# Optimization experiments

Measured on AMD Instinct MI355X. Metric: run time of the kernel, lower is better.

The kernel has to match this reference:

```python
import jax, jax.numpy as jnp
import numpy as np

N, F = 16384, 32
H1, H2, D1, D2 = 64, 64, 32, 1


def setup_inputs() -> dict:
    key = jax.random.key(0)
    ks = jax.random.split(key, 10)
    x = jax.random.normal(ks[0], (N, F), dtype=jnp.float32)
    # pre-normalized adjacency (GCNConv expects D^-1/2 A D^-1/2); mimic with uniform/N
    a = jax.random.uniform(ks[1], (N, N), dtype=jnp.float32) / N
    # glorot-ish scaled params
    W1 = jax.random.normal(ks[2], (F, H1), dtype=jnp.float32) * (1.0 / np.sqrt(F))
    b1 = jnp.zeros((H1,), dtype=jnp.float32)
    W2 = jax.random.normal(ks[3], (H1, H2), dtype=jnp.float32) * (1.0 / np.sqrt(H1))
    b2 = jnp.zeros((H2,), dtype=jnp.float32)
    Wd1 = jax.random.normal(ks[4], (H2, D1), dtype=jnp.float32) * (1.0 / np.sqrt(H2))
    bd1 = jnp.zeros((D1,), dtype=jnp.float32)
    Wd2 = jax.random.normal(ks[5], (D1, D2), dtype=jnp.float32) * (1.0 / np.sqrt(D1))
    bd2 = jnp.zeros((D2,), dtype=jnp.float32)
    return {"x": x, "a": a, "W1": W1, "b1": b1, "W2": W2, "b2": b2,
            "Wd1": Wd1, "bd1": bd1, "Wd2": Wd2, "bd2": bd2}


def reference(x, a, W1, b1, W2, b2, Wd1, bd1, Wd2, bd2):
    # GCNConv: relu(a @ (x @ W) + b)   (a is pre-normalized)
    g1 = jax.nn.relu(a @ (x @ W1) + b1)   # [N, 64]
    g2 = jax.nn.relu(a @ (g1 @ W2) + b2)  # [N, 64]
    d3 = jax.nn.relu(g2 @ Wd1 + bd1)      # [N, 32]
    return d3 @ Wd2 + bd2                 # [N, 1]
```

## Files before the change

### kernel.cpp

```cpp
#include <hip/hip_runtime.h>
#include <hip/hip_bf16.h>


typedef __bf16 bf16x8 __attribute__((ext_vector_type(8)));
typedef float  f32x16 __attribute__((ext_vector_type(16)));
typedef float  f32x4v __attribute__((ext_vector_type(4)));
typedef int    i32x4  __attribute__((ext_vector_type(4)));

#define NNODE 16384
#define KDIM  16384
#define HCOL  64

__device__ inline i32x4 pack8(f32x4v a, f32x4v b){
  bf16x8 t;
  t[0]=(__bf16)a[0]; t[1]=(__bf16)a[1]; t[2]=(__bf16)a[2]; t[3]=(__bf16)a[3];
  t[4]=(__bf16)b[0]; t[5]=(__bf16)b[1]; t[6]=(__bf16)b[2]; t[7]=(__bf16)b[3];
  return __builtin_bit_cast(i32x4, t);
}

__global__ __launch_bounds__(128) void gcn_layer_kernel(
    const float* __restrict__ A,
    const __bf16* __restrict__ Ht,
    const float* __restrict__ bias,
    float* __restrict__ G)
{
  __shared__ i32x4 sA[2*2*256];
  __shared__ i32x4 sH[2*2*512];

  const int tid  = threadIdx.x;
  const int lane = tid & 63;
  const int kw   = tid >> 6;
  const int row0 = blockIdx.x * 32;

  const int rA0  = lane >> 3;
  const int ccA  = lane & 7;
  const int swzA = ccA ^ rA0;
  const int r    = lane & 31;
  const int hsub = lane >> 5;
  const int xs   = lane & 7;

  const size_t k0base = (size_t)kw * 8192;

  f32x4v ra[8]; i32x4 rh[8];

  const float* pA0 = A + (size_t)(row0 + rA0) * KDIM + k0base + (size_t)ccA*8;
  const i32x4* pH0 = (const i32x4*)Ht + (size_t)rA0 * (KDIM/8) + k0base/8 + ccA;

  auto stage_load = [&](int t){
    const float* pA = pA0 + (size_t)t*64;
    #pragma unroll
    for (int pi=0; pi<4; ++pi){
      const float* p = pA + (size_t)pi*8*KDIM;
      ra[2*pi]   = __builtin_nontemporal_load((const f32x4v*)p);
      ra[2*pi+1] = __builtin_nontemporal_load((const f32x4v*)(p+4));
    }
    const i32x4* pH = pH0 + (size_t)t*8;
    #pragma unroll
    for (int pi=0; pi<8; ++pi)
      rh[pi] = pH[(size_t)pi*8*(KDIM/8)];
  };

  auto stage_write = [&](int buf){
    i32x4* dA = &sA[(kw*2+buf)*256];
    #pragma unroll
    for (int pi=0; pi<4; ++pi)
      dA[(rA0 + pi*8)*8 + swzA] = pack8(ra[2*pi], ra[2*pi+1]);
    i32x4* dH = &sH[(kw*2+buf)*512];
    #pragma unroll
    for (int pi=0; pi<8; ++pi)
      dH[(rA0 + pi*8)*8 + swzA] = rh[pi];
  };

  f32x16 acc0 = {}; f32x16 acc1 = {};

  auto compute = [&](int buf){
    const i32x4* bA = &sA[(kw*2+buf)*256];
    const i32x4* bH = &sH[(kw*2+buf)*512];
    #pragma unroll
    for (int kk=0; kk<4; ++kk){
      int c = (kk*2 + hsub) ^ xs;
      bf16x8 a  = __builtin_bit_cast(bf16x8, bA[r*8 + c]);
      bf16x8 b0 = __builtin_bit_cast(bf16x8, bH[r*8 + c]);
      bf16x8 b1 = __builtin_bit_cast(bf16x8, bH[(r+32)*8 + c]);
      acc0 = __builtin_amdgcn_mfma_f32_32x32x16_bf16(a, b0, acc0, 0,0,0);
      acc1 = __builtin_amdgcn_mfma_f32_32x32x16_bf16(a, b1, acc1, 0,0,0);
    }
  };

  stage_load(0);
  stage_write(0);
  stage_load(1);

  #pragma unroll 1
  for (int t=0; t<127; ++t){
    int nx = t+2; if (nx > 127) nx = 127;
    compute(t&1);
    stage_write((t+1)&1);
    stage_load(nx);
  }
  compute(1);

  __syncthreads();

  float* red = (float*)sA;
  if (kw == 1){
    #pragma unroll
    for (int j=0; j<16; ++j){
      int rr = (j&3) + 8*(j>>2) + 4*hsub;
      red[rr*64 + r]      = acc0[j];
      red[rr*64 + 32 + r] = acc1[j];
    }
  }
  __syncthreads();
  if (kw == 0){
    #pragma unroll
    for (int j=0; j<16; ++j){
      int rr = (j&3) + 8*(j>>2) + 4*hsub;
      float v0 = acc0[j] + red[rr*64 + r]      + bias[r];
      float v1 = acc1[j] + red[rr*64 + 32 + r] + bias[32 + r];
      G[(size_t)(row0 + rr)*HCOL + r]      = fmaxf(v0, 0.f);
      G[(size_t)(row0 + rr)*HCOL + 32 + r] = fmaxf(v1, 0.f);
    }
  }
}

template<int F>
__global__ __launch_bounds__(128) void proj_T_kernel(
    const float* __restrict__ in,
    const float* __restrict__ W,
    __bf16* __restrict__ out)
{
  constexpr int FP = F + 4;
  __shared__ float sWt[64*FP];
  __shared__ short sOut[64*136];

  int tid = threadIdx.x;
  for (int e = tid; e < 64*F; e += 128){
    int h = e / F, j = e - h*F;
    sWt[h*FP + j] = W[j*64 + h];
  }
  __syncthreads();

  const size_t n = (size_t)blockIdx.x*128 + tid;
  float rowv[F];
  #pragma unroll
  for (int j=0; j<F; j+=4){
    f32x4v v = *(const f32x4v*)(in + n*F + j);
    rowv[j]=v[0]; rowv[j+1]=v[1]; rowv[j+2]=v[2]; rowv[j+3]=v[3];
  }
  #pragma unroll
  for (int h=0; h<64; ++h){
    float s = 0.f;
    #pragma unroll
    for (int j=0; j<F; j+=4){
      f32x4v w = *(const f32x4v*)&sWt[h*FP + j];
      s += rowv[j]*w[0] + rowv[j+1]*w[1] + rowv[j+2]*w[2] + rowv[j+3]*w[3];
    }
    sOut[h*136 + tid] = __builtin_bit_cast(short, (__bf16)s);
  }
  __syncthreads();

  const size_t n0 = (size_t)blockIdx.x*128;
  #pragma unroll
  for (int pi=0; pi<8; ++pi){
    int p = pi*128 + tid;
    int h = p >> 4, cc = p & 15;
    i32x4 v = *(const i32x4*)&sOut[h*136 + cc*8];
    *(i32x4*)(out + (size_t)h*NNODE + n0 + cc*8) = v;
  }
}

__global__ __launch_bounds__(256) void tail_kernel(
    const float* __restrict__ g2,
    const float* __restrict__ Wd1,
    const float* __restrict__ bd1,
    const float* __restrict__ Wd2,
    const float* __restrict__ bd2,
    float* __restrict__ outp)
{
  __shared__ float sW[64*32];
  __shared__ float sb1[32], sw2[32];
  int tid = threadIdx.x;
  for (int e=tid; e<2048; e+=256) sW[e] = Wd1[e];
  if (tid < 32){ sb1[tid] = bd1[tid]; sw2[tid] = Wd2[tid]; }
  __syncthreads();

  size_t n = (size_t)blockIdx.x*256 + tid;
  float rv[64];
  #pragma unroll
  for (int j=0;j<64;j+=4){
    f32x4v v = *(const f32x4v*)(g2 + n*64 + j);
    rv[j]=v[0]; rv[j+1]=v[1]; rv[j+2]=v[2]; rv[j+3]=v[3];
  }
  float o = 0.f;
  #pragma unroll
  for (int c=0;c<32;++c){
    float s = sb1[c];
    #pragma unroll
    for (int j=0;j<64;++j) s += rv[j]*sW[j*32 + c];
    o += fmaxf(s, 0.f) * sw2[c];
  }
  outp[n] = o + bd2[0];
}

extern "C" void kernel_launch(void* const* d_in, const int* in_sizes, int n_in,
                              void* d_out, int out_size, void* d_ws, size_t ws_size,
                              hipStream_t stream)
{
  const float* x   = (const float*)d_in[0];
  const float* a   = (const float*)d_in[1];
  const float* W1  = (const float*)d_in[2];
  const float* b1  = (const float*)d_in[3];
  const float* W2  = (const float*)d_in[4];
  const float* b2  = (const float*)d_in[5];
  const float* Wd1 = (const float*)d_in[6];
  const float* bd1 = (const float*)d_in[7];
  const float* Wd2 = (const float*)d_in[8];
  const float* bd2 = (const float*)d_in[9];
  float* outp = (float*)d_out;

  char* ws = (char*)d_ws;
  __bf16* Ht1 = (__bf16*)(ws);
  __bf16* Ht2 = (__bf16*)(ws + (2u<<20));
  float*  g1  = (float*)(ws + (4u<<20));
  float*  g2  = (float*)(ws + (8u<<20));

  proj_T_kernel<32><<<128, 128, 0, stream>>>(x,  W1, Ht1);
  gcn_layer_kernel <<<512, 128, 0, stream>>>(a, Ht1, b1, g1);
  proj_T_kernel<64><<<128, 128, 0, stream>>>(g1, W2, Ht2);
  gcn_layer_kernel <<<512, 128, 0, stream>>>(a, Ht2, b2, g2);
  tail_kernel      <<<64, 256, 0, stream>>>(g2, Wd1, bd1, Wd2, bd2, outp);
}
```

Baseline: 509.4 us.

## Double row tile to 64 and split K across four waves in GCN layer

```diff
diff --git a/kernel.cpp b/kernel.cpp
--- a/kernel.cpp
+++ b/kernel.cpp
@@ -17,39 +17,40 @@
   t[4]=(__bf16)b[0]; t[5]=(__bf16)b[1]; t[6]=(__bf16)b[2]; t[7]=(__bf16)b[3];
   return __builtin_bit_cast(i32x4, t);
 }
-
-__global__ __launch_bounds__(128) void gcn_layer_kernel(
+#define BC(x) __builtin_bit_cast(bf16x8, x)
+
+__global__ __launch_bounds__(256, 1) void gcn_layer_kernel(
     const float* __restrict__ A,
     const __bf16* __restrict__ Ht,
     const float* __restrict__ bias,
     float* __restrict__ G)
 {
-  __shared__ i32x4 sA[2*2*256];
-  __shared__ i32x4 sH[2*2*512];
+  __shared__ i32x4 sA[4*2*512];
+  __shared__ i32x4 sH[4*2*512];
 
   const int tid  = threadIdx.x;
   const int lane = tid & 63;
   const int kw   = tid >> 6;
-  const int row0 = blockIdx.x * 32;
+  const int row0 = blockIdx.x * 64;
 
   const int rA0  = lane >> 3;
   const int ccA  = lane & 7;
   const int swzA = ccA ^ rA0;
   const int r    = lane & 31;
   const int hsub = lane >> 5;
-  const int xs   = lane & 7;
-
-  const size_t k0base = (size_t)kw * 8192;
-
-  f32x4v ra[8]; i32x4 rh[8];
-
-  const float* pA0 = A + (size_t)(row0 + rA0) * KDIM + k0base + (size_t)ccA*8;
-  const i32x4* pH0 = (const i32x4*)Ht + (size_t)rA0 * (KDIM/8) + k0base/8 + ccA;
+  const int xs   = r & 7;
+
+  const size_t k0 = (size_t)kw * 4096;
+
+  f32x4v ra[16]; i32x4 rh[8];
+
+  const float* pA0 = A + (size_t)(row0 + rA0) * KDIM + k0 + (size_t)ccA*8;
+  const i32x4* pH0 = (const i32x4*)Ht + (size_t)rA0 * (KDIM/8) + k0/8 + ccA;
 
   auto stage_load = [&](int t){
     const float* pA = pA0 + (size_t)t*64;
     #pragma unroll
-    for (int pi=0; pi<4; ++pi){
+    for (int pi=0; pi<8; ++pi){
       const float* p = pA + (size_t)pi*8*KDIM;
       ra[2*pi]   = __builtin_nontemporal_load((const f32x4v*)p);
       ra[2*pi+1] = __builtin_nontemporal_load((const f32x4v*)(p+4));
@@ -61,9 +62,9 @@
   };
 
   auto stage_write = [&](int buf){
-    i32x4* dA = &sA[(kw*2+buf)*256];
-    #pragma unroll
-    for (int pi=0; pi<4; ++pi)
+    i32x4* dA = &sA[(kw*2+buf)*512];
+    #pragma unroll
+    for (int pi=0; pi<8; ++pi)
       dA[(rA0 + pi*8)*8 + swzA] = pack8(ra[2*pi], ra[2*pi+1]);
     i32x4* dH = &sH[(kw*2+buf)*512];
     #pragma unroll
@@ -71,44 +72,48 @@
       dH[(rA0 + pi*8)*8 + swzA] = rh[pi];
   };
 
-  f32x16 acc0 = {}; f32x16 acc1 = {};
+  f32x16 acc00 = {}, acc01 = {}, acc10 = {}, acc11 = {};
 
   auto compute = [&](int buf){
-    const i32x4* bA = &sA[(kw*2+buf)*256];
+    const i32x4* bA = &sA[(kw*2+buf)*512];
     const i32x4* bH = &sH[(kw*2+buf)*512];
     #pragma unroll
     for (int kk=0; kk<4; ++kk){
       int c = (kk*2 + hsub) ^ xs;
-      bf16x8 a  = __builtin_bit_cast(bf16x8, bA[r*8 + c]);
-      bf16x8 b0 = __builtin_bit_cast(bf16x8, bH[r*8 + c]);
-      bf16x8 b1 = __builtin_bit_cast(bf16x8, bH[(r+32)*8 + c]);
-      acc0 = __builtin_amdgcn_mfma_f32_32x32x16_bf16(a, b0, acc0, 0,0,0);
-      acc1 = __builtin_amdgcn_mfma_f32_32x32x16_bf16(a, b1, acc1, 0,0,0);
+      bf16x8 a0 = BC(bA[r*8 + c]);
+      bf16x8 a1 = BC(bA[(r+32)*8 + c]);
+      bf16x8 b0 = BC(bH[r*8 + c]);
+      bf16x8 b1 = BC(bH[(r+32)*8 + c]);
+      acc00 = __builtin_amdgcn_mfma_f32_32x32x16_bf16(a0, b0, acc00, 0,0,0);
+      acc01 = __builtin_amdgcn_mfma_f32_32x32x16_bf16(a0, b1, acc01, 0,0,0);
+      acc10 = __builtin_amdgcn_mfma_f32_32x32x16_bf16(a1, b0, acc10, 0,0,0);
+      acc11 = __builtin_amdgcn_mfma_f32_32x32x16_bf16(a1, b1, acc11, 0,0,0);
     }
   };
 
   stage_load(0);
   stage_write(0);
   stage_load(1);
-
   #pragma unroll 1
-  for (int t=0; t<127; ++t){
-    int nx = t+2; if (nx > 127) nx = 127;
+  for (int t=0; t<63; ++t){
     compute(t&1);
     stage_write((t+1)&1);
-    stage_load(nx);
+    if (t < 62) stage_load(t+2);
   }
   compute(1);
 
   __syncthreads();
 
   float* red = (float*)sA;
-  if (kw == 1){
+  if (kw > 0){
+    float* rd = red + (size_t)(kw-1)*4096;
     #pragma unroll
     for (int j=0; j<16; ++j){
       int rr = (j&3) + 8*(j>>2) + 4*hsub;
-      red[rr*64 + r]      = acc0[j];
-      red[rr*64 + 32 + r] = acc1[j];
+      rd[(rr   )*64 + r]      = acc00[j];
+      rd[(rr   )*64 + 32 + r] = acc01[j];
+      rd[(rr+32)*64 + r]      = acc10[j];
+      rd[(rr+32)*64 + 32 + r] = acc11[j];
     }
   }
   __syncthreads();
@@ -116,10 +121,14 @@
     #pragma unroll
     for (int j=0; j<16; ++j){
       int rr = (j&3) + 8*(j>>2) + 4*hsub;
-      float v0 = acc0[j] + red[rr*64 + r]      + bias[r];
-      float v1 = acc1[j] + red[rr*64 + 32 + r] + bias[32 + r];
-      G[(size_t)(row0 + rr)*HCOL + r]      = fmaxf(v0, 0.f);
-      G[(size_t)(row0 + rr)*HCOL + 32 + r] = fmaxf(v1, 0.f);
+      float v00 = acc00[j] + red[(rr   )*64+r]    + red[4096+(rr   )*64+r]    + red[8192+(rr   )*64+r]    + bias[r];
+      float v01 = acc01[j] + red[(rr   )*64+32+r] + red[4096+(rr   )*64+32+r] + red[8192+(rr   )*64+32+r] + bias[32+r];
+      float v10 = acc10[j] + red[(rr+32)*64+r]    + red[4096+(rr+32)*64+r]    + red[8192+(rr+32)*64+r]    + bias[r];
+      float v11 = acc11[j] + red[(rr+32)*64+32+r] + red[4096+(rr+32)*64+32+r] + red[8192+(rr+32)*64+32+r] + bias[32+r];
+      G[(size_t)(row0 + rr     )*HCOL + r]      = fmaxf(v00, 0.f);
+      G[(size_t)(row0 + rr     )*HCOL + 32 + r] = fmaxf(v01, 0.f);
+      G[(size_t)(row0 + rr + 32)*HCOL + r]      = fmaxf(v10, 0.f);
+      G[(size_t)(row0 + rr + 32)*HCOL + 32 + r] = fmaxf(v11, 0.f);
     }
   }
 }
@@ -226,8 +235,8 @@
   float*  g2  = (float*)(ws + (8u<<20));
 
   proj_T_kernel<32><<<128, 128, 0, stream>>>(x,  W1, Ht1);
-  gcn_layer_kernel <<<512, 128, 0, stream>>>(a, Ht1, b1, g1);
+  gcn_layer_kernel <<<256, 256, 0, stream>>>(a, Ht1, b1, g1);
   proj_T_kernel<64><<<128, 128, 0, stream>>>(g1, W2, Ht2);
-  gcn_layer_kernel <<<512, 128, 0, stream>>>(a, Ht2, b2, g2);
+  gcn_layer_kernel <<<256, 256, 0, stream>>>(a, Ht2, b2, g2);
   tail_kernel      <<<64, 256, 0, stream>>>(g2, Wd1, bd1, Wd2, bd2, outp);
 }
```

Result: faster. 453.8 us (-10.9%).
